# Kernel optimization log

Measured on AMD Instinct MI355X. Metric: run time of the kernel, lower is better.

Reference implementation:

```python
import jax, jax.numpy as jnp
import numpy as np

EPS = 1e-6

def _normalize(x, axis):
    # torch F.normalize with eps: x / max(||x||_2, eps)
    n = jnp.linalg.norm(x, axis=axis, keepdims=True)
    return x / jnp.maximum(n, EPS)

def setup_inputs() -> dict:
    key = jax.random.key(0)
    ks = jax.random.split(key, 6)
    B, C, H, W = 16, 512, 32, 32
    N, D = 16384, 32
    return {
        "encodings": jax.random.normal(ks[0], (B, C, H, W), dtype=jnp.float32),
        "emb_weight": jax.random.normal(ks[1], (N, D), dtype=jnp.float32),
        "proj_w": jax.random.normal(ks[2], (D, C), dtype=jnp.float32) * 0.05,
        "proj_b": jax.random.normal(ks[3], (D,), dtype=jnp.float32) * 0.05,
        "exp_w": jax.random.normal(ks[4], (C, D), dtype=jnp.float32) * 0.05,
        "exp_b": jax.random.normal(ks[5], (C,), dtype=jnp.float32) * 0.05,
    }

def reference(encodings, emb_weight, proj_w, proj_b, exp_w, exp_b):
    N = emb_weight.shape[0]
    # projection: 1x1 conv == channel matmul; z: [B, D, H, W]
    z = jnp.einsum('bchw,dc->bdhw', encodings, proj_w) + proj_b[None, :, None, None]
    z = _normalize(z, axis=1)
    e = _normalize(emb_weight, axis=1)  # [N, D]
    # cosine similarities [B, N, H, W] -> nearest code per position
    sims = jnp.einsum('bdhw,nd->bnhw', z, e)
    idx = jnp.argmax(sims, axis=1)  # [B, H, W] int
    latents = jnp.transpose(e[idx], (0, 3, 1, 2))  # [B, D, H, W]
    loss_quantization = jnp.mean(jnp.square(z - latents))
    # straight-through estimator
    latents = z + jax.lax.stop_gradient(latents - z)
    out = jnp.einsum('bdhw,cd->bchw', latents, exp_w) + exp_b[None, :, None, None]
    # usage histogram -> perplexity
    flat = idx.ravel()
    usages = jnp.zeros((N,), dtype=jnp.float32).at[flat].add(1.0) / flat.shape[0]
    perplexity = jnp.exp(jnp.sum(-usages * jnp.log(usages + 1e-6)))
    return out, loss_quantization, perplexity
```

## Files before the change

### kernel.cpp

```cpp
#include <hip/hip_runtime.h>
#include <cstdint>

#define BATCH   16
#define CCH     512
#define DD      32
#define NCODES  16384
#define HWSZ    1024
#define P_TOTAL 16384
#define NCHUNK  32
#define CHUNK   (NCODES / NCHUNK)

typedef _Float16 half8 __attribute__((ext_vector_type(8)));
typedef float    f32x4 __attribute__((ext_vector_type(4)));

union H8 { _Float16 h[8]; uint4 u; };
union L8 { uint4 u; half8 h; };


__global__ __launch_bounds__(256) void prep_kernel(
    const float* __restrict__ enc, const float* __restrict__ pw,
    const float* __restrict__ pb, const float* __restrict__ emb,
    float* __restrict__ z, float* __restrict__ invz, char* __restrict__ zf16,
    float* __restrict__ en, char* __restrict__ ef16,
    int* __restrict__ hist, float* __restrict__ scalarAcc)
{
    const int t = threadIdx.x;

    if (blockIdx.x >= 320) {
        const int i = (blockIdx.x - 320) * 256 + t;
        hist[i] = 0;
        if (blockIdx.x == 320 && t < 4) scalarAcc[t] = 0.f;
        return;
    }

    if (blockIdx.x >= 256) {
        const int r = (blockIdx.x - 256) * 256 + t;
        const float4* src = reinterpret_cast<const float4*>(emb + (size_t)r * DD);
        float4 v[8];
        float ssq = 0.f;
#pragma unroll
        for (int q = 0; q < 8; q++) {
            v[q] = src[q];
            ssq += v[q].x * v[q].x + v[q].y * v[q].y + v[q].z * v[q].z + v[q].w * v[q].w;
        }
        const float inv = 1.f / fmaxf(sqrtf(ssq), 1e-6f);
        float4* dst = reinterpret_cast<float4*>(en + (size_t)r * DD);
        char* row = ef16 + (size_t)r * 128;
#pragma unroll
        for (int q = 0; q < 8; q += 2) {
            H8 hi, lo;
#pragma unroll
            for (int u = 0; u < 2; u++) {
                float4 o;
                o.x = v[q + u].x * inv; o.y = v[q + u].y * inv;
                o.z = v[q + u].z * inv; o.w = v[q + u].w * inv;
                dst[q + u] = o;
                const float s[4] = {o.x * 4096.f, o.y * 4096.f, o.z * 4096.f, o.w * 4096.f};
#pragma unroll
                for (int j = 0; j < 4; j++) {
                    const _Float16 h = (_Float16)s[j];
                    hi.h[u * 4 + j] = h;
                    lo.h[u * 4 + j] = (_Float16)(s[j] - (float)h);
                }
            }
            *(uint4*)(row + q * 8)      = hi.u;
            *(uint4*)(row + 64 + q * 8) = lo.u;
        }
        return;
    }

    const int hw_l = t & 63;
    const int dg   = __builtin_amdgcn_readfirstlane(t >> 6);
    const int p0   = blockIdx.x * 64;
    const int b    = p0 >> 10;
    const int hw   = (p0 & 1023) + hw_l;
    const float* encb = enc + (size_t)b * (CCH * HWSZ) + hw;

    float acc[8];
#pragma unroll
    for (int j = 0; j < 8; j++) acc[j] = 0.f;

    float ev[16];
#pragma unroll
    for (int u = 0; u < 16; u++) ev[u] = encb[(size_t)u * HWSZ];

    for (int c0 = 0; c0 < CCH - 16; c0 += 16) {
        float nv[16];
#pragma unroll
        for (int u = 0; u < 16; u++)
            nv[u] = encb[(size_t)(c0 + 16 + u) * HWSZ];
#pragma unroll
        for (int u = 0; u < 16; u++)
#pragma unroll
            for (int j = 0; j < 8; j++)
                acc[j] = fmaf(ev[u], pw[(dg * 8 + j) * CCH + c0 + u], acc[j]);
#pragma unroll
        for (int u = 0; u < 16; u++) ev[u] = nv[u];
    }
#pragma unroll
    for (int u = 0; u < 16; u++)
#pragma unroll
        for (int j = 0; j < 8; j++)
            acc[j] = fmaf(ev[u], pw[(dg * 8 + j) * CCH + (CCH - 16) + u], acc[j]);

    const int p = p0 + hw_l;
    float ssq = 0.f;
    H8 hi, lo;
#pragma unroll
    for (int j = 0; j < 8; j++) {
        const float v = acc[j] + pb[dg * 8 + j];
        z[(size_t)p * DD + dg * 8 + j] = v;
        ssq = fmaf(v, v, ssq);
        const float vs = v * 4096.f;
        const _Float16 h = (_Float16)vs;
        hi.h[j] = h;
        lo.h[j] = (_Float16)(vs - (float)h);
    }
    char* row = zf16 + (size_t)p * 128;
    *(uint4*)(row + dg * 16)      = hi.u;
    *(uint4*)(row + 64 + dg * 16) = lo.u;

    __shared__ float red[4][64];
    red[dg][hw_l] = ssq;
    __syncthreads();
    if (t < 64) {
        const float tot = red[0][t] + red[1][t] + red[2][t] + red[3][t];
        invz[p0 + t] = 1.f / fmaxf(sqrtf(tot), 1e-6f);
    }
}

__global__ __launch_bounds__(256, 4) void argmax_kernel(
    const char* __restrict__ zf16, const char* __restrict__ ef16,
    float* __restrict__ pval, int* __restrict__ pidx)
{
    const int w    = threadIdx.x >> 6;
    const int lane = threadIdx.x & 63;
    const int col  = lane & 15;
    const int quad = lane >> 4;
    const int chunk = (blockIdx.x & 7) * 4 + (blockIdx.x >> 9);
    const int pg    = (blockIdx.x >> 3) & 63;
    const int wp0   = pg * 256 + w * 64;

    half8 bh[4], bl[4];
#pragma unroll
    for (int tt = 0; tt < 4; tt++) {
        const char* r = zf16 + (size_t)(wp0 + tt * 16 + col) * 128 + quad * 16;
        L8 a; a.u = *(const uint4*)(r);       bh[tt] = a.h;
        L8 b; b.u = *(const uint4*)(r + 64);  bl[tt] = b.h;
    }

    const int n0 = chunk * CHUNK;
    const char* abase = ef16 + (size_t)(n0 + col) * 128 + quad * 16;

    float best[4] = {-3e38f, -3e38f, -3e38f, -3e38f};
    int   bidx[4] = {0, 0, 0, 0};
    int   code = n0 + quad * 4;

    uint4 p0h = *(const uint4*)(abase);
    uint4 p0l = *(const uint4*)(abase + 64);
    uint4 p1h = *(const uint4*)(abase + 2048);
    uint4 p1l = *(const uint4*)(abase + 2048 + 64);
    const f32x4 zero4 = {0.f, 0.f, 0.f, 0.f};

    for (int tile = 0; tile < CHUNK / 16; tile++) {
        L8 ahu, alu;
        ahu.u = p0h;
        alu.u = p0l;
        p0h = p1h; p0l = p1l;
        const char* nxt = abase + (size_t)(tile + 2) * 2048;
        p1h = *(const uint4*)(nxt);
        p1l = *(const uint4*)(nxt + 64);

        const half8 ah = ahu.h, al = alu.h;

        f32x4 acc[4];
#pragma unroll
        for (int tt = 0; tt < 4; tt++)
            acc[tt] = __builtin_amdgcn_mfma_f32_16x16x32_f16(ah, bh[tt], zero4, 0, 0, 0);
#pragma unroll
        for (int tt = 0; tt < 4; tt++)
            acc[tt] = __builtin_amdgcn_mfma_f32_16x16x32_f16(ah, bl[tt], acc[tt], 0, 0, 0);
#pragma unroll
        for (int tt = 0; tt < 4; tt++)
            acc[tt] = __builtin_amdgcn_mfma_f32_16x16x32_f16(al, bh[tt], acc[tt], 0, 0, 0);
#pragma unroll
        for (int tt = 0; tt < 4; tt++)
            acc[tt] = __builtin_amdgcn_mfma_f32_16x16x32_f16(al, bl[tt], acc[tt], 0, 0, 0);

#pragma unroll
        for (int tt = 0; tt < 4; tt++)
#pragma unroll
            for (int r = 0; r < 4; r++) {
                const float v = acc[tt][r];
                if (v > best[tt]) { best[tt] = v; bidx[tt] = code + r; }
            }
        code += 16;
    }

#pragma unroll
    for (int off = 16; off < 64; off <<= 1) {
#pragma unroll
        for (int tt = 0; tt < 4; tt++) {
            const float ov = __shfl_xor(best[tt], off);
            const int   oi = __shfl_xor(bidx[tt], off);
            if (ov > best[tt] || (ov == best[tt] && oi < bidx[tt])) {
                best[tt] = ov; bidx[tt] = oi;
            }
        }
    }
    if (quad == 0) {
#pragma unroll
        for (int tt = 0; tt < 4; tt++) {
            pval[(size_t)chunk * P_TOTAL + wp0 + tt * 16 + col] = best[tt];
            pidx[(size_t)chunk * P_TOTAL + wp0 + tt * 16 + col] = bidx[tt];
        }
    }
}

__global__ __launch_bounds__(512) void combex_kernel(
    const float* __restrict__ pval, const int* __restrict__ pidx,
    const float* __restrict__ z, const float* __restrict__ invz,
    const float* __restrict__ en, const float* __restrict__ ew,
    const float* __restrict__ eb,
    int* __restrict__ hist, float* __restrict__ scalarAcc,
    float* __restrict__ out)
{
    const int t  = threadIdx.x;
    const int p0 = blockIdx.x * 64;

    __shared__ float lat[64 * 33];
    __shared__ float bvs[8][64];
    __shared__ int   bis[8][64];

    {
        const int pl = t & 63;
        const int kg = t >> 6;
        const int p  = p0 + pl;
        float best = -3e38f;
        int   bi   = 0;
#pragma unroll
        for (int k = 0; k < 4; k++) {
            const float v = pval[(size_t)(kg * 4 + k) * P_TOTAL + p];
            const int   i = pidx[(size_t)(kg * 4 + k) * P_TOTAL + p];
            if (v > best) { best = v; bi = i; }
        }
        bvs[kg][pl] = best;
        bis[kg][pl] = bi;
    }
    __syncthreads();

    if (t < 64) {
        float best = bvs[0][t];
        int   bi   = bis[0][t];
#pragma unroll
        for (int kg = 1; kg < 8; kg++) {
            const float v = bvs[kg][t];
            const int   i = bis[kg][t];
            if (v > best || (v == best && i < bi)) { best = v; bi = i; }
        }
        const int p = p0 + t;
        atomicAdd(&hist[bi], 1);

        const float iv = invz[p];
        const float4* zsrc = reinterpret_cast<const float4*>(z + (size_t)p * DD);
        const float4* esrc = reinterpret_cast<const float4*>(en + (size_t)bi * DD);
        float ls = 0.f;
#pragma unroll
        for (int q = 0; q < 8; q++) {
            const float4 zv = zsrc[q];
            const float4 ev = esrc[q];
            lat[t * 33 + q * 4 + 0] = ev.x;
            lat[t * 33 + q * 4 + 1] = ev.y;
            lat[t * 33 + q * 4 + 2] = ev.z;
            lat[t * 33 + q * 4 + 3] = ev.w;
            const float dx = zv.x * iv - ev.x;
            const float dy = zv.y * iv - ev.y;
            const float dz = zv.z * iv - ev.z;
            const float dw = zv.w * iv - ev.w;
            ls += dx * dx + dy * dy + dz * dz + dw * dw;
        }
#pragma unroll
        for (int off = 32; off > 0; off >>= 1) ls += __shfl_down(ls, off);
        if (t == 0) atomicAdd(&scalarAcc[0], ls);
    }
    __syncthreads();

    const int hw_l = t & 63;
    const int cg   = __builtin_amdgcn_readfirstlane(t >> 6);
    float lr[32];
#pragma unroll
    for (int d = 0; d < DD; d++) lr[d] = lat[hw_l * 33 + d];

    const int b   = p0 >> 10;
    const int hw0 = p0 & 1023;
    float* outb = out + (size_t)b * (CCH * HWSZ) + hw0 + hw_l;
    const int c0 = cg * 64;
#pragma unroll 4
    for (int k = 0; k < 64; k++) {
        const int c = c0 + k;
        const float* ewc = ew + (size_t)c * DD;
        float s0 = 0.f, s1 = 0.f, s2 = 0.f, s3 = 0.f;
#pragma unroll
        for (int d = 0; d < DD; d += 4) {
            s0 = fmaf(lr[d + 0], ewc[d + 0], s0);
            s1 = fmaf(lr[d + 1], ewc[d + 1], s1);
            s2 = fmaf(lr[d + 2], ewc[d + 2], s2);
            s3 = fmaf(lr[d + 3], ewc[d + 3], s3);
        }
        outb[(size_t)c * HWSZ] = (s0 + s1) + (s2 + s3) + eb[c];
    }
}

__global__ __launch_bounds__(256) void entropy_kernel(
    const int* __restrict__ hist, float* __restrict__ scalarAcc,
    float* __restrict__ out_scalars)
{
    const int i = blockIdx.x * 256 + threadIdx.x;
    const float u = (float)hist[i] * (1.f / (float)P_TOTAL);
    float h = -u * logf(u + 1e-6f);
    __shared__ float red[256];
    red[threadIdx.x] = h;
    __syncthreads();
    for (int s = 128; s > 0; s >>= 1) {
        if (threadIdx.x < s) red[threadIdx.x] += red[threadIdx.x + s];
        __syncthreads();
    }
    if (threadIdx.x == 0) {
        atomicAdd(&scalarAcc[1], red[0]);
        __threadfence();
        int* cnt = (int*)(scalarAcc + 2);
        const int prev = atomicAdd(cnt, 1);
        if (prev == 63) {
            const float loss = __hip_atomic_load(&scalarAcc[0], __ATOMIC_RELAXED,
                                                 __HIP_MEMORY_SCOPE_AGENT);
            const float ent  = __hip_atomic_load(&scalarAcc[1], __ATOMIC_RELAXED,
                                                 __HIP_MEMORY_SCOPE_AGENT);
            out_scalars[0] = loss * (1.f / (float)(P_TOTAL * DD));
            out_scalars[1] = expf(ent);
        }
    }
}

extern "C" void kernel_launch(void* const* d_in, const int* in_sizes, int n_in,
                              void* d_out, int out_size, void* d_ws, size_t ws_size,
                              hipStream_t stream)
{
    const float* enc = (const float*)d_in[0];
    const float* emb = (const float*)d_in[1];
    const float* pw  = (const float*)d_in[2];
    const float* pb  = (const float*)d_in[3];
    const float* ew  = (const float*)d_in[4];
    const float* eb  = (const float*)d_in[5];
    float* out = (float*)d_out;

    char* ws = (char*)d_ws;
    float* z         = (float*)(ws + 0);
    float* invz      = (float*)(ws + 2097152);
    float* en        = (float*)(ws + 2162688);
    char*  zf16      = ws + 4259840;
    char*  ef16      = ws + 6356992;
    float* pval      = (float*)(ws + 8454144);
    int*   pidx      = (int*)  (ws + 10551296);
    int*   hist      = (int*)  (ws + 12648448);
    float* scalarAcc = (float*)(ws + 12713984);

    prep_kernel   <<<384, 256, 0, stream>>>(enc, pw, pb, emb, z, invz, zf16,
                                            en, ef16, hist, scalarAcc);
    argmax_kernel <<<64 * NCHUNK, 256, 0, stream>>>(zf16, ef16, pval, pidx);
    combex_kernel <<<P_TOTAL / 64, 512, 0, stream>>>(pval, pidx, z, invz, en,
                                                     ew, eb, hist, scalarAcc, out);
    entropy_kernel<<<NCODES / 256, 256, 0, stream>>>(hist, scalarAcc,
                                                     out + 8388608);
}
```

Measured before the change: 252.2 us.

## Unroll argmax over four code tiles per round and halve code chunks

The argmax kernel now processes 64 codes per iteration, four 16-code tiles with a 4x4 MFMA accumulator array and whole-round prefetch, where it previously handled one 16-code tile per iteration. The number of code chunks drops from 32 to 16, so each block scans twice as many codes and the combine kernel reads half as many partial results. The aim is more independent MFMA work per loop iteration to hide issue latency, and less partial-result traffic. The cost is much higher register use: the occupancy hint is removed, the grid is halved, and the block index mapping changes to a plain point-group by chunk order.

```diff
diff --git a/kernel.cpp b/kernel.cpp
--- a/kernel.cpp
+++ b/kernel.cpp
@@ -7,7 +7,7 @@
 #define NCODES  16384
 #define HWSZ    1024
 #define P_TOTAL 16384
-#define NCHUNK  32
+#define NCHUNK  16
 #define CHUNK   (NCODES / NCHUNK)
 
 typedef _Float16 half8 __attribute__((ext_vector_type(8)));
@@ -129,7 +129,7 @@
     }
 }
 
-__global__ __launch_bounds__(256, 4) void argmax_kernel(
+__global__ __launch_bounds__(256) void argmax_kernel(
     const char* __restrict__ zf16, const char* __restrict__ ef16,
     float* __restrict__ pval, int* __restrict__ pidx)
 {
@@ -137,8 +137,8 @@
     const int lane = threadIdx.x & 63;
     const int col  = lane & 15;
     const int quad = lane >> 4;
-    const int chunk = (blockIdx.x & 7) * 4 + (blockIdx.x >> 9);
-    const int pg    = (blockIdx.x >> 3) & 63;
+    const int pg    = blockIdx.x & 63;
+    const int chunk = blockIdx.x >> 6;
     const int wp0   = pg * 256 + w * 64;
 
     half8 bh[4], bl[4];
@@ -152,49 +152,70 @@
     const int n0 = chunk * CHUNK;
     const char* abase = ef16 + (size_t)(n0 + col) * 128 + quad * 16;
 
-    float best[4] = {-3e38f, -3e38f, -3e38f, -3e38f};
-    int   bidx[4] = {0, 0, 0, 0};
-    int   code = n0 + quad * 4;
-
-    uint4 p0h = *(const uint4*)(abase);
-    uint4 p0l = *(const uint4*)(abase + 64);
-    uint4 p1h = *(const uint4*)(abase + 2048);
-    uint4 p1l = *(const uint4*)(abase + 2048 + 64);
+    float best[4]  = {-3e38f, -3e38f, -3e38f, -3e38f};
+    int   bcode[4] = {0, 0, 0, 0};
     const f32x4 zero4 = {0.f, 0.f, 0.f, 0.f};
 
-    for (int tile = 0; tile < CHUNK / 16; tile++) {
-        L8 ahu, alu;
-        ahu.u = p0h;
-        alu.u = p0l;
-        p0h = p1h; p0l = p1l;
-        const char* nxt = abase + (size_t)(tile + 2) * 2048;
-        p1h = *(const uint4*)(nxt);
-        p1l = *(const uint4*)(nxt + 64);
-
-        const half8 ah = ahu.h, al = alu.h;
-
-        f32x4 acc[4];
-#pragma unroll
-        for (int tt = 0; tt < 4; tt++)
-            acc[tt] = __builtin_amdgcn_mfma_f32_16x16x32_f16(ah, bh[tt], zero4, 0, 0, 0);
-#pragma unroll
-        for (int tt = 0; tt < 4; tt++)
-            acc[tt] = __builtin_amdgcn_mfma_f32_16x16x32_f16(ah, bl[tt], acc[tt], 0, 0, 0);
-#pragma unroll
-        for (int tt = 0; tt < 4; tt++)
-            acc[tt] = __builtin_amdgcn_mfma_f32_16x16x32_f16(al, bh[tt], acc[tt], 0, 0, 0);
-#pragma unroll
-        for (int tt = 0; tt < 4; tt++)
-            acc[tt] = __builtin_amdgcn_mfma_f32_16x16x32_f16(al, bl[tt], acc[tt], 0, 0, 0);
-
-#pragma unroll
-        for (int tt = 0; tt < 4; tt++)
-#pragma unroll
-            for (int r = 0; r < 4; r++) {
-                const float v = acc[tt][r];
-                if (v > best[tt]) { best[tt] = v; bidx[tt] = code + r; }
+    uint4 cah[4], cal[4];
+#pragma unroll
+    for (int it = 0; it < 4; it++) {
+        cah[it] = *(const uint4*)(abase + it * 2048);
+        cal[it] = *(const uint4*)(abase + it * 2048 + 64);
+    }
+
+    for (int rnd = 0; rnd < CHUNK / 64; rnd++) {
+        const char* nb = abase + (size_t)(rnd + 1) * 8192;
+        uint4 nah[4], nal[4];
+#pragma unroll
+        for (int it = 0; it < 4; it++) {
+            nah[it] = *(const uint4*)(nb + it * 2048);
+            nal[it] = *(const uint4*)(nb + it * 2048 + 64);
+        }
+
+        half8 ah[4], al[4];
+#pragma unroll
+        for (int it = 0; it < 4; it++) {
+            L8 x; x.u = cah[it]; ah[it] = x.h;
+            L8 y; y.u = cal[it]; al[it] = y.h;
+        }
+
+        f32x4 acc[4][4];
+#pragma unroll
+        for (int it = 0; it < 4; it++)
+#pragma unroll
+            for (int tt = 0; tt < 4; tt++)
+                acc[it][tt] = __builtin_amdgcn_mfma_f32_16x16x32_f16(ah[it], bh[tt], zero4, 0, 0, 0);
+#pragma unroll
+        for (int it = 0; it < 4; it++)
+#pragma unroll
+            for (int tt = 0; tt < 4; tt++)
+                acc[it][tt] = __builtin_amdgcn_mfma_f32_16x16x32_f16(ah[it], bl[tt], acc[it][tt], 0, 0, 0);
+#pragma unroll
+        for (int it = 0; it < 4; it++)
+#pragma unroll
+            for (int tt = 0; tt < 4; tt++)
+                acc[it][tt] = __builtin_amdgcn_mfma_f32_16x16x32_f16(al[it], bh[tt], acc[it][tt], 0, 0, 0);
+#pragma unroll
+        for (int it = 0; it < 4; it++)
+#pragma unroll
+            for (int tt = 0; tt < 4; tt++)
+                acc[it][tt] = __builtin_amdgcn_mfma_f32_16x16x32_f16(al[it], bl[tt], acc[it][tt], 0, 0, 0);
+
+#pragma unroll
+        for (int it = 0; it < 4; it++) {
+            const int base = n0 + (rnd * 4 + it) * 16 + quad * 4;
+#pragma unroll
+            for (int tt = 0; tt < 4; tt++) {
+                const f32x4 a = acc[it][tt];
+#pragma unroll
+                for (int r = 0; r < 4; r++) {
+                    if (a[r] > best[tt]) { best[tt] = a[r]; bcode[tt] = base + r; }
+                }
             }
-        code += 16;
+        }
+
+#pragma unroll
+        for (int it = 0; it < 4; it++) { cah[it] = nah[it]; cal[it] = nal[it]; }
     }
 
 #pragma unroll
@@ -202,9 +223,9 @@
 #pragma unroll
         for (int tt = 0; tt < 4; tt++) {
             const float ov = __shfl_xor(best[tt], off);
-            const int   oi = __shfl_xor(bidx[tt], off);
-            if (ov > best[tt] || (ov == best[tt] && oi < bidx[tt])) {
-                best[tt] = ov; bidx[tt] = oi;
+            const int   oi = __shfl_xor(bcode[tt], off);
+            if (ov > best[tt] || (ov == best[tt] && oi < bcode[tt])) {
+                best[tt] = ov; bcode[tt] = oi;
             }
         }
     }
@@ -212,7 +233,7 @@
 #pragma unroll
         for (int tt = 0; tt < 4; tt++) {
             pval[(size_t)chunk * P_TOTAL + wp0 + tt * 16 + col] = best[tt];
-            pidx[(size_t)chunk * P_TOTAL + wp0 + tt * 16 + col] = bidx[tt];
+            pidx[(size_t)chunk * P_TOTAL + wp0 + tt * 16 + col] = bcode[tt];
         }
     }
 }
@@ -239,9 +260,9 @@
         float best = -3e38f;
         int   bi   = 0;
 #pragma unroll
-        for (int k = 0; k < 4; k++) {
-            const float v = pval[(size_t)(kg * 4 + k) * P_TOTAL + p];
-            const int   i = pidx[(size_t)(kg * 4 + k) * P_TOTAL + p];
+        for (int k = 0; k < 2; k++) {
+            const float v = pval[(size_t)(kg * 2 + k) * P_TOTAL + p];
+            const int   i = pidx[(size_t)(kg * 2 + k) * P_TOTAL + p];
             if (v > best) { best = v; bi = i; }
         }
         bvs[kg][pl] = best;
@@ -360,9 +381,9 @@
     char*  zf16      = ws + 4259840;
     char*  ef16      = ws + 6356992;
     float* pval      = (float*)(ws + 8454144);
-    int*   pidx      = (int*)  (ws + 10551296);
-    int*   hist      = (int*)  (ws + 12648448);
-    float* scalarAcc = (float*)(ws + 12713984);
+    int*   pidx      = (int*)  (ws + 9502720);
+    int*   hist      = (int*)  (ws + 10551296);
+    float* scalarAcc = (float*)(ws + 10616832);
 
     prep_kernel   <<<384, 256, 0, stream>>>(enc, pw, pb, emb, z, invz, zf16,
                                             en, ef16, hist, scalarAcc);
```

Measured after the change: 268.0 us. +6.3%, slower.
